# Optimization experiments

Hardware: AMD Instinct MI355X
Metric: run time of the kernel (lower is better)

Reference implementation:

```python
import jax, jax.numpy as jnp
import numpy as np

SIGMA = 1.0          # influence distance of kernel points
KERNEL_RADIUS = 1.0  # radius within which kernel points live


def setup_inputs() -> dict:
    key = jax.random.key(0)
    k0, k1, k2, k3, k4 = jax.random.split(key, 5)
    B, M, K_NB, D_IN, D_OUT, K_PTS = 4, 16384, 32, 64, 64, 15
    X = jax.random.normal(k0, (B, M, 3), dtype=jnp.float32)          # point coords
    F = jax.random.normal(k1, (B, M, D_IN), dtype=jnp.float32)        # point features
    N = jax.random.randint(k2, (B, M, K_NB), 0, M)                    # neighbor indices
    Q = jax.random.uniform(k3, (K_PTS, 3), minval=-KERNEL_RADIUS,
                           maxval=KERNEL_RADIUS, dtype=jnp.float32)   # kernel points
    W = jax.random.normal(k4, (K_PTS, D_IN, D_OUT), dtype=jnp.float32) * 0.05
    return {"X": X, "F": F, "N": N, "Q": Q, "W": W}


def reference(X, F, N, Q, W):
    # Gather neighbor coordinates and features: [B, M, k, 3] / [B, M, k, d_in]
    gather = jax.vmap(lambda a, idx: a[idx])
    Xn = gather(X, N)
    Fn = gather(F, N)
    # Relative neighbor positions w.r.t. each center point
    r = Xn - X[:, :, None, :]                                  # [B, M, k, 3]
    # Distance of each relative position to each kernel point
    d = jnp.linalg.norm(r[:, :, :, None, :] - Q, axis=-1)      # [B, M, k, Kp]
    # Linear correlation influence (KPConv)
    h = jnp.maximum(0.0, 1.0 - d / SIGMA)                      # [B, M, k, Kp]
    # Distance-weighted neighbor aggregation per kernel point
    Fk = jnp.einsum('bmkp,bmkd->bmpd', h, Fn)                  # [B, M, Kp, d_in]
    # Per-kernel-point linear maps, summed over kernel points
    return jnp.einsum('bmpd,pde->bme', Fk, W)                  # [B, M, d_out]
```

## Files before the change

kernel.cpp:

```cpp
#include <hip/hip_runtime.h>
#include <hip/hip_bf16.h>


#define BATCH 4
#define MPTS  16384
#define KNB   32
#define DIN   64
#define DOUT  64
#define KP    15
#define K2P   1024
#define KSTEPS (K2P/32)
#define ROWB  (K2P*2)
#define PTS   (BATCH*MPTS)
#define PPB   16
#define NBLK  (PTS/PPB)
#define WBELEMS (K2P*DOUT)

typedef __bf16 bf16x8 __attribute__((ext_vector_type(8)));
typedef float  f32x4  __attribute__((ext_vector_type(4)));
typedef unsigned short u16x8 __attribute__((ext_vector_type(8)));

static __device__ __forceinline__ unsigned short f2b(float x) {
    __bf16 h = (__bf16)x;
    return __builtin_bit_cast(unsigned short, h);
}

__global__ void prep_wb(const float* __restrict__ W, unsigned short* __restrict__ wb) {
    int idx = blockIdx.x * 256 + threadIdx.x;
    if (idx >= WBELEMS) return;
    int i    = idx & 7;
    int lane = (idx >> 3) & 63;
    int ks   = (idx >> 9) & 31;
    int et   = idx >> 14;
    int kap  = ks * 32 + ((lane >> 4) << 3) + i;
    int n = kap >> 6;
    int g = (kap >> 4) & 3;
    int t = (kap >> 2) & 3;
    int r = kap & 3;
    int p = g * 4 + r;
    int d = n * 4 + t;
    int e = et * 16 + (lane & 15);
    float v = (p < KP) ? W[(p * DIN + d) * DOUT + e] : 0.f;
    wb[idx] = f2b(v);
}

__global__ void f2bf_kernel(const float* __restrict__ src, unsigned short* __restrict__ dst, int n8) {
    int i = blockIdx.x * 256 + threadIdx.x;
    if (i >= n8) return;
    const float4* s = reinterpret_cast<const float4*>(src) + (size_t)i * 2;
    float4 a = s[0], b = s[1];
    u16x8 o;
    o[0] = f2b(a.x); o[1] = f2b(a.y); o[2] = f2b(a.z); o[3] = f2b(a.w);
    o[4] = f2b(b.x); o[5] = f2b(b.y); o[6] = f2b(b.z); o[7] = f2b(b.w);
    *(reinterpret_cast<u16x8*>(dst) + i) = o;
}

__global__ __launch_bounds__(256, 4)
void kpconv_main(const float* __restrict__ X, const unsigned short* __restrict__ FB,
                 const int* __restrict__ NB, const float* __restrict__ Q,
                 const unsigned short* __restrict__ WB, float* __restrict__ OUT) {
    __shared__ unsigned short fk[16 * K2P];
    __shared__ float4 stg[4][4][KNB];

    const int tid  = threadIdx.x;
    const int wv   = tid >> 6;
    const int lane = tid & 63;
    const int g16  = lane >> 4;
    const int r16  = lane & 15;

    float qx = 1.0e3f, qy = 0.f, qz = 0.f;
    if (r16 < KP) { qx = Q[r16 * 3 + 0]; qy = Q[r16 * 3 + 1]; qz = Q[r16 * 3 + 2]; }

    const int bid     = blockIdx.x;
    const int base_pt = (bid & 7) * (PTS / 8) + (bid >> 3) * PPB;

    #pragma unroll
    for (int e = 0; e < 2; ++e) {
        int ent = lane + e * 64;
        int j = ent >> 5, k = ent & 31;
        int pid = base_pt + wv * 4 + j;
        int b   = pid >> 14;
        int nb  = NB[(size_t)pid * KNB + k];
        int gidx = b * MPTS + nb;
        const float* xn = X + (size_t)gidx * 3;
        const float* xc = X + (size_t)pid * 3;
        float4 v;
        v.x = xn[0] - xc[0];
        v.y = xn[1] - xc[1];
        v.z = xn[2] - xc[2];
        v.w = __int_as_float(gidx);
        int slot = (k & 24) | ((k ^ (k >> 3)) & 7);
        stg[wv][j][slot] = v;
    }

    #pragma unroll
    for (int j = 0; j < 4; ++j) {
        const int row = wv * 4 + j;

        float4 rv[8];
        #pragma unroll
        for (int i = 0; i < 8; ++i)
            rv[i] = stg[wv][j][g16 * 8 + (i ^ g16)];

        union U { uint2 d; unsigned short s[4]; };
        U L[8];
        #pragma unroll
        for (int i = 0; i < 8; ++i) {
            int gi = __float_as_int(rv[i].w);
            L[i].d = *reinterpret_cast<const uint2*>(FB + ((size_t)gi << 6) + (r16 << 2));
        }

        bf16x8 ah;
        #pragma unroll
        for (int i = 0; i < 8; ++i) {
            float dx = rv[i].x - qx, dy = rv[i].y - qy, dz = rv[i].z - qz;
            float d2 = fmaf(dx, dx, fmaf(dy, dy, dz * dz));
            ah[i] = (__bf16)fmaxf(1.f - sqrtf(d2), 0.f);
        }

        const f32x4 z = {0.f, 0.f, 0.f, 0.f};
        f32x4 accs[4];
        #pragma unroll
        for (int t = 0; t < 4; ++t) {
            bf16x8 bf;
            #pragma unroll
            for (int i = 0; i < 8; ++i)
                bf[i] = __builtin_bit_cast(__bf16, L[i].s[t]);
            accs[t] = __builtin_amdgcn_mfma_f32_16x16x32_bf16(ah, bf, z, 0, 0, 0);
        }

        bf16x8 w0, w1;
        #pragma unroll
        for (int r = 0; r < 4; ++r) {
            w0[r]     = (__bf16)accs[0][r];
            w0[4 + r] = (__bf16)accs[1][r];
            w1[r]     = (__bf16)accs[2][r];
            w1[4 + r] = (__bf16)accs[3][r];
        }
        int swz  = (row & 7) ^ (r16 & 7);
        int off0 = row * ROWB + (r16 * 8 + ((g16 * 2 + 0) ^ swz)) * 16;
        int off1 = row * ROWB + (r16 * 8 + ((g16 * 2 + 1) ^ swz)) * 16;
        *reinterpret_cast<bf16x8*>(reinterpret_cast<char*>(fk) + off0) = w0;
        *reinterpret_cast<bf16x8*>(reinterpret_cast<char*>(fk) + off1) = w1;
    }

    __syncthreads();

    const unsigned short* wbp = WB + ((size_t)(wv * KSTEPS) * 64 + lane) * 8;
    asm volatile("" : "+v"(wbp));

    f32x4 o = {0.f, 0.f, 0.f, 0.f};
    #pragma unroll
    for (int ks = 0; ks < KSTEPS; ++ks) {
        bf16x8 b = *reinterpret_cast<const bf16x8*>(wbp + ks * 512);
        int stored = (ks * 4 + g16) ^ (r16 & 7) ^ ((ks >> 1) & 7);
        bf16x8 a = *reinterpret_cast<const bf16x8*>(
            reinterpret_cast<const char*>(fk) + r16 * ROWB + stored * 16);
        o = __builtin_amdgcn_mfma_f32_16x16x32_bf16(a, b, o, 0, 0, 0);
    }

    #pragma unroll
    for (int r = 0; r < 4; ++r) {
        int pid = base_pt + g16 * 4 + r;
        OUT[(size_t)pid * DOUT + wv * 16 + r16] = o[r];
    }
}

extern "C" void kernel_launch(void* const* d_in, const int* in_sizes, int n_in,
                              void* d_out, int out_size, void* d_ws, size_t ws_size,
                              hipStream_t stream) {
    const float* X = (const float*)d_in[0];
    const float* F = (const float*)d_in[1];
    const int*   N = (const int*)d_in[2];
    const float* Q = (const float*)d_in[3];
    const float* W = (const float*)d_in[4];
    float* OUT = (float*)d_out;
    unsigned short* WB = (unsigned short*)d_ws;
    unsigned short* FB = WB + WBELEMS;

    prep_wb<<<(WBELEMS + 255) / 256, 256, 0, stream>>>(W, WB);

    const int n8 = PTS * DIN / 8;
    f2bf_kernel<<<(n8 + 255) / 256, 256, 0, stream>>>(F, FB, n8);

    kpconv_main<<<NBLK, 256, 0, stream>>>(X, FB, N, Q, WB, OUT);
}
```

Measured before the change: 66.01 us.

## Prefetch neighbor feature gathers two rows ahead and expand distance algebraically

```diff
diff --git a/kernel.cpp b/kernel.cpp
--- a/kernel.cpp
+++ b/kernel.cpp
@@ -70,64 +70,75 @@
 
     float qx = 1.0e3f, qy = 0.f, qz = 0.f;
     if (r16 < KP) { qx = Q[r16 * 3 + 0]; qy = Q[r16 * 3 + 1]; qz = Q[r16 * 3 + 2]; }
+    const float qq   = qx * qx + qy * qy + qz * qz;
+    const float nq2x = -2.f * qx, nq2y = -2.f * qy, nq2z = -2.f * qz;
 
     const int bid     = blockIdx.x;
     const int base_pt = (bid & 7) * (PTS / 8) + (bid >> 3) * PPB;
+    const int boff    = (base_pt >> 14) * MPTS;
+    const int pid0    = base_pt + wv * 4;
 
     #pragma unroll
     for (int e = 0; e < 2; ++e) {
         int ent = lane + e * 64;
         int j = ent >> 5, k = ent & 31;
-        int pid = base_pt + wv * 4 + j;
-        int b   = pid >> 14;
+        int pid = pid0 + j;
         int nb  = NB[(size_t)pid * KNB + k];
-        int gidx = b * MPTS + nb;
+        int gidx = boff + nb;
         const float* xn = X + (size_t)gidx * 3;
         const float* xc = X + (size_t)pid * 3;
-        float4 v;
-        v.x = xn[0] - xc[0];
-        v.y = xn[1] - xc[1];
-        v.z = xn[2] - xc[2];
-        v.w = __int_as_float(gidx);
+        float rx = xn[0] - xc[0];
+        float ry = xn[1] - xc[1];
+        float rz = xn[2] - xc[2];
+        float rr = fmaf(rx, rx, fmaf(ry, ry, rz * rz));
         int slot = (k & 24) | ((k ^ (k >> 3)) & 7);
-        stg[wv][j][slot] = v;
+        stg[wv][j][slot] = make_float4(rx, ry, rz, rr);
     }
+
+    union U { uint2 d; unsigned short s[4]; };
+    U L[2][8];
+
+    auto issue_gather = [&](int j, U* Lj) {
+        const int* nbp = NB + (size_t)(pid0 + j) * KNB + g16 * 8;
+        int4 a = *reinterpret_cast<const int4*>(nbp);
+        int4 b = *reinterpret_cast<const int4*>(nbp + 4);
+        int g[8] = {a.x, a.y, a.z, a.w, b.x, b.y, b.z, b.w};
+        #pragma unroll
+        for (int i = 0; i < 8; ++i)
+            Lj[i].d = *reinterpret_cast<const uint2*>(
+                FB + ((size_t)(boff + g[i]) << 6) + (r16 << 2));
+    };
+
+    issue_gather(0, L[0]);
+    issue_gather(1, L[1]);
 
     #pragma unroll
     for (int j = 0; j < 4; ++j) {
         const int row = wv * 4 + j;
 
-        float4 rv[8];
-        #pragma unroll
-        for (int i = 0; i < 8; ++i)
-            rv[i] = stg[wv][j][g16 * 8 + (i ^ g16)];
-
-        union U { uint2 d; unsigned short s[4]; };
-        U L[8];
-        #pragma unroll
-        for (int i = 0; i < 8; ++i) {
-            int gi = __float_as_int(rv[i].w);
-            L[i].d = *reinterpret_cast<const uint2*>(FB + ((size_t)gi << 6) + (r16 << 2));
-        }
-
         bf16x8 ah;
         #pragma unroll
         for (int i = 0; i < 8; ++i) {
-            float dx = rv[i].x - qx, dy = rv[i].y - qy, dz = rv[i].z - qz;
-            float d2 = fmaf(dx, dx, fmaf(dy, dy, dz * dz));
-            ah[i] = (__bf16)fmaxf(1.f - sqrtf(d2), 0.f);
+            float4 rv = stg[wv][j][g16 * 8 + (i ^ g16)];
+            float d2 = fmaf(rv.x, nq2x, fmaf(rv.y, nq2y, fmaf(rv.z, nq2z, rv.w + qq)));
+            d2 = fmaxf(d2, 0.f);
+            ah[i] = (__bf16)fmaxf(1.f - __builtin_amdgcn_sqrtf(d2), 0.f);
         }
+
+        bf16x8 bfr[4];
+        #pragma unroll
+        for (int t = 0; t < 4; ++t)
+            #pragma unroll
+            for (int i = 0; i < 8; ++i)
+                bfr[t][i] = __builtin_bit_cast(__bf16, L[j & 1][i].s[t]);
+
+        if (j < 2) issue_gather(j + 2, L[j & 1]);
 
         const f32x4 z = {0.f, 0.f, 0.f, 0.f};
         f32x4 accs[4];
         #pragma unroll
-        for (int t = 0; t < 4; ++t) {
-            bf16x8 bf;
-            #pragma unroll
-            for (int i = 0; i < 8; ++i)
-                bf[i] = __builtin_bit_cast(__bf16, L[i].s[t]);
-            accs[t] = __builtin_amdgcn_mfma_f32_16x16x32_bf16(ah, bf, z, 0, 0, 0);
-        }
+        for (int t = 0; t < 4; ++t)
+            accs[t] = __builtin_amdgcn_mfma_f32_16x16x32_bf16(ah, bfr[t], z, 0, 0, 0);
 
         bf16x8 w0, w1;
         #pragma unroll
```

Result: faster. 63.45 us (-3.9%).
